# Kernel tuning notes

Measured on AMD Instinct MI355X. Metric: run time of the kernel, lower is better.

The kernel has to match this reference:

```python
import jax, jax.numpy as jnp
import numpy as np

T, D, N, K, V = 4, 1024, 256, 64, 32000
SGLD_A, SGLD_B, SGLD_C = 0.01, 1.0, 0.55
PHI_VAR, ETA_VAR = 1.0, 1.0
ZERO = 1e-6

def jax_exp(x):
    return jnp.clip(jnp.exp(jnp.clip(x, -700.0, 700.0)), ZERO)

def setup_inputs() -> dict:
    key = jax.random.key(0)
    ks = jax.random.split(key, 13)
    W = jax.random.randint(ks[0], (T, D, N), 0, V, dtype=jnp.int32)
    Z = jax.random.randint(ks[1], (T, D, N), 0, K - 1, dtype=jnp.int32)
    prop_word_idx = jax.random.randint(ks[2], (T, D, N), 0, N, dtype=jnp.int32)
    prop_topic = jax.random.randint(ks[3], (T, D, N), 0, K - 1, dtype=jnp.int32)
    u_mh = jax.random.uniform(ks[4], (T, D, N, 2), dtype=jnp.float32)
    noise_eta = jax.random.normal(ks[5], (T, D), dtype=jnp.float32)
    noise_phi = jax.random.normal(ks[6], (T,), dtype=jnp.float32)
    alpha = jax.random.normal(ks[7], (T, K), dtype=jnp.float32)
    phi = jax.random.normal(ks[8], (T, V, K), dtype=jnp.float32) * 0.1
    eta = jax.random.normal(ks[9], (T, D, K), dtype=jnp.float32) * 0.1
    CDK = jax.random.uniform(ks[10], (T, D, K), dtype=jnp.float32) * (N / K)
    CWK = jax.random.uniform(ks[11], (T, V, K), dtype=jnp.float32)
    CK = jax.random.uniform(ks[12], (T, K), dtype=jnp.float32) * (D * N / K)
    return dict(W=W, Z=Z, prop_word_idx=prop_word_idx, prop_topic=prop_topic,
                u_mh=u_mh, noise_eta=noise_eta, noise_phi=noise_phi,
                alpha=alpha, phi=phi, eta=eta, CDK=CDK, CWK=CWK, CK=CK)

def reference(W, Z, prop_word_idx, prop_topic, u_mh, noise_eta, noise_phi,
              alpha, phi, eta, CDK, CWK, CK):
    eps = SGLD_A * (SGLD_B + 0.0) ** (-SGLD_C)  # SGLD step at iteration 0

    # --- SGLD update of eta (per doc), vmapped over (T, D) via broadcasting ---
    prior_eta = (alpha[:, None, :] - eta) / ETA_VAR                 # [T,D,K]
    grad_eta = CDK - N * jax.nn.softmax(eta, axis=-1)               # [T,D,K]
    eta_new = eta + eps / 2 * (grad_eta + prior_eta) + noise_eta[..., None] * eps

    tt = jnp.arange(T)[:, None, None]   # [T,1,1]
    dd = jnp.arange(D)[None, :, None]   # [1,D,1]

    # --- MH step 1: word-proposal (acceptance via phi ratio) ---
    pre = Z                                                           # [T,D,N]
    prop1 = jnp.take_along_axis(Z, prop_word_idx, axis=2)             # [T,D,N]
    a1 = jax_exp(phi[tt, W, prop1]) / jax_exp(phi[tt, W, pre])
    k1 = jnp.where(u_mh[..., 0] < a1, prop1, pre)

    # --- MH step 2: topic-proposal (acceptance via eta ratio) ---
    a2 = jax_exp(eta_new[tt, dd, prop_topic]) / jax_exp(eta_new[tt, dd, k1])
    z_new = jnp.where(u_mh[..., 1] < a2, prop_topic, k1)              # [T,D,N]

    # --- scatter counter updates (add new assignment, remove old) ---
    CDK_new = CDK.at[tt, dd, z_new].add(1.0).at[tt, dd, Z].add(-1.0)
    CWK_new = CWK.at[tt, W, z_new].add(1.0).at[tt, W, Z].add(-1.0)
    CK_new = CK.at[tt, z_new].add(1.0).at[tt, Z].add(-1.0)

    # --- SGLD update of phi: sequential over T (reads updated phi[t-1]) ---
    rows = [phi[t] for t in range(T)]   # each [V,K]
    phi_sigma = 1.0 / (1.0 / 100.0 + 1.0 / PHI_VAR)
    for t in range(T):
        if t == 0:
            prior = (2.0 * phi[1] * (phi_sigma / PHI_VAR) - 2.0 * rows[0]) / PHI_VAR
        elif t == T - 1:
            prior = (rows[t - 1] - rows[t]) / PHI_VAR
        else:
            prior = (phi[t + 1] + rows[t - 1] - 2.0 * rows[t]) / PHI_VAR
        grad = CWK_new[t] - CK_new[t][None, :] * jax.nn.softmax(rows[t], axis=0)
        rows[t] = rows[t] + eps / 2 * (grad + prior) + noise_phi[t] * eps
    phi_new = jnp.stack(rows)

    return (eta_new, phi_new, CDK_new, CWK_new, CK_new, z_new)
```

## Files before the change

kernel.cpp:

```cpp
#include <hip/hip_runtime.h>

#define T 4
#define D 1024
#define NN 256
#define K 64
#define V 32000
#define VK (V*K)
#define TD (T*D)
#define NB 32
#define CAP 1024

__device__ __forceinline__ float jexp(float x) {
    x = fminf(fmaxf(x, -700.0f), 700.0f);
    return fmaxf(expf(x), 1e-6f);
}


__global__ void fused_kernel(const int* __restrict__ W, const int* __restrict__ Z,
                             const int* __restrict__ pwi, const int* __restrict__ ptop,
                             const float* __restrict__ u, const float* __restrict__ phi,
                             const float* __restrict__ eta,
                             const float* __restrict__ alpha,
                             const float* __restrict__ noise_eta,
                             const float* __restrict__ CDK,
                             const float* __restrict__ CK,
                             float* __restrict__ S_part,
                             float* __restrict__ CK_new,
                             float* __restrict__ eta_new,
                             float* __restrict__ CDK_new,
                             unsigned int* __restrict__ resv,
                             unsigned int* __restrict__ list,
                             float* __restrict__ z_out)
{
    int blk = blockIdx.x;
    int n = threadIdx.x;

    __shared__ float sm[256];
    __shared__ float esh[K];
    __shared__ int   hist[K];
    __shared__ int   bcnt[NB];
    __shared__ int   bbase[NB];

    if (blk < 500) {
        if (blk == 0) CK_new[n] = CK[n];
        int t = blk / 125;
        int vbase = (blk % 125) * 256;
        int k = n & 63;
        int rr = n >> 6;
        const float* base = phi + (size_t)t * VK;
        float s = 0.0f;
        #pragma unroll 4
        for (int it = 0; it < 64; ++it) {
            int v = vbase + it * 4 + rr;
            s += expf(base[v * K + k]);
        }
        sm[n] = s;
        __syncthreads();
        if (n < 64) {
            S_part[blk * 64 + n] = sm[n] + sm[n + 64] +
                                   sm[n + 128] + sm[n + 192];
        }
        return;
    }

    int b = blk - 500;
    int r = ((b & 7) << 9) | (b >> 3);
    int t = r >> 10;
    int slice = (b >> 3) & 15;

    int w     = W[r * NN + n];
    int pre   = Z[r * NN + n];
    int pw    = pwi[r * NN + n];
    int prop1 = Z[r * NN + pw];
    int pt    = ptop[r * NN + n];
    float2 uu = ((const float2*)u)[(size_t)r * NN + n];

    const float* prow = phi + ((size_t)t * V + w) * K;
    float f1 = prow[prop1];
    float f0 = prow[pre];

    float cdk = 0.0f;
    if (n < 64) {
        float x = eta[r * K + n];
        float m = x;
        #pragma unroll
        for (int off = 32; off >= 1; off >>= 1)
            m = fmaxf(m, __shfl_xor(m, off, 64));
        float e = expf(x - m);
        float s = e;
        #pragma unroll
        for (int off = 32; off >= 1; off >>= 1)
            s += __shfl_xor(s, off, 64);
        float smx = e / s;
        cdk = CDK[r * K + n];
        float grad  = cdk - (float)NN * smx;
        float prior = alpha[t * K + n] - x;
        float en = x + 0.005f * (grad + prior) + noise_eta[r] * 0.01f;
        esh[n] = en;
        eta_new[r * K + n] = en;
    } else if (n < 128) {
        hist[n - 64] = 0;
    } else if (n < 128 + NB) {
        bcnt[n - 128] = 0;
    }
    __syncthreads();

    float a1 = jexp(f1) / jexp(f0);
    int k1 = (uu.x < a1) ? prop1 : pre;

    float a2 = jexp(esh[pt]) / jexp(esh[k1]);
    int z = (uu.y < a2) ? pt : k1;

    atomicAdd(&hist[z], 1);
    atomicAdd(&hist[pre], -1);

    int keep = (z != pre);
    int bucket = w / 1000;
    int myidx = 0;
    if (keep) myidx = atomicAdd(&bcnt[bucket], 1);
    __syncthreads();

    if (n < NB) {
        bbase[n] = (int)atomicAdd(&resv[(t * NB + n) * 16 + slice],
                                  (unsigned int)bcnt[n]);
    }
    __syncthreads();

    z_out[r * NN + n] = (float)z;
    if (keep) {
        int slot = bbase[bucket] + myidx;
        if (slot < CAP) {
            unsigned int pk = (unsigned int)w | ((unsigned int)z << 15) |
                              ((unsigned int)pre << 21);
            list[(size_t)((t * NB + bucket) * 16 + slice) * CAP + slot] = pk;
        }
    }
    if (n < K) {
        CDK_new[r * K + n] = cdk + (float)hist[n];
    }
}

__global__ void cwk_kernel(const unsigned int* __restrict__ list,
                           const unsigned int* __restrict__ resv,
                           const float* __restrict__ CWK,
                           float* __restrict__ CWK_new)
{
    int b = blockIdx.x;
    int xcd    = b & 7;
    int tbh    = (b >> 3) & 15;
    int window = b >> 7;
    int tb = tbh * 8 + xcd;
    int t = tb >> 5, bucket = tb & 31;
    int vbase = bucket * 1000 + window * 125;

    __shared__ unsigned int plusH[125 * 16];
    __shared__ unsigned int minusH[125 * 16];
    for (int i = threadIdx.x; i < 2000; i += 256) { plusH[i] = 0u; minusH[i] = 0u; }
    __syncthreads();

    int wave = threadIdx.x >> 6;
    int lane = threadIdx.x & 63;
    int segbase = tb * 16;

#define DECODE(PK) {                                                        \
        int wv = (int)((PK) & 32767u);                                      \
        unsigned int vl = (unsigned int)(wv - vbase);                       \
        if (vl < 125u) {                                                    \
            int zz = (int)(((PK) >> 15) & 63u);                             \
            int pr = (int)(((PK) >> 21) & 63u);                             \
            atomicAdd(&plusH [vl * 16 + (zz >> 2)], 1u << ((zz & 3) * 8));  \
            atomicAdd(&minusH[vl * 16 + (pr >> 2)], 1u << ((pr & 3) * 8));  \
        } }

    for (int s = wave; s < 16; s += 4) {
        int len = (int)resv[segbase + s]; if (len > CAP) len = CAP;
        const unsigned int* lp = list + (size_t)(segbase + s) * CAP;
        const uint4* lp4 = (const uint4*)lp;
        int n4 = len >> 2;
        for (int i = lane; i < n4; i += 64) {
            uint4 q = lp4[i];
            DECODE(q.x); DECODE(q.y); DECODE(q.z); DECODE(q.w);
        }
        int base4 = n4 << 2;
        if (lane < (len & 3)) { unsigned int pk = lp[base4 + lane]; DECODE(pk); }
    }
#undef DECODE
    __syncthreads();

    const float4* src = (const float4*)(CWK     + ((size_t)t * V + vbase) * 64);
    float4*       dst = (float4*)      (CWK_new + ((size_t)t * V + vbase) * 64);
    for (int i4 = threadIdx.x; i4 < 2000; i4 += 256) {
        unsigned int pl = plusH[i4];
        unsigned int mi = minusH[i4];
        float4 c = src[i4];
        float4 o;
        #pragma unroll
        for (int jj = 0; jj < 4; ++jj) {
            int sh = jj * 8;
            (&o.x)[jj] = (&c.x)[jj] + (float)((pl >> sh) & 255u)
                                    - (float)((mi >> sh) & 255u);
        }
        dst[i4] = o;
    }
}

__global__ void reduce_kernel(const float* __restrict__ S_part,
                              const float* __restrict__ CDKn,
                              const float* __restrict__ CDK,
                              float* __restrict__ S,
                              float* __restrict__ CK_new)
{
    int b = blockIdx.x;
    int tid = threadIdx.x;

    if (b < 4 && tid < 64) {
        float s = 0.0f;
        #pragma unroll 5
        for (int i = 0; i < 125; ++i)
            s += S_part[(b * 125 + i) * 64 + tid];
        S[b * 64 + tid] = s;
    }

    int t  = b >> 4;
    int k  = tid & 63;
    int dl = tid >> 6;
    int dbase = (b & 15) << 6;
    float s = 0.0f;
    #pragma unroll
    for (int i = 0; i < 16; ++i) {
        int d = dbase + dl + (i << 2);
        size_t idx = ((size_t)(t << 10) + d) * 64 + k;
        s += CDKn[idx] - CDK[idx];
    }
    __shared__ float sm[256];
    sm[tid] = s;
    __syncthreads();
    if (tid < 64) {
        float tot = sm[k] + sm[k + 64] + sm[k + 128] + sm[k + 192];
        if (tot != 0.0f) atomicAdd(&CK_new[(t << 6) + k], tot);
    }
}

__global__ void phi_update_kernel(const float* __restrict__ phi,
                                  const float* __restrict__ CWKn,
                                  const float* __restrict__ CKn,
                                  const float* __restrict__ S,
                                  const float* __restrict__ noise_phi,
                                  float* __restrict__ phi_new)
{
    int i4 = blockIdx.x * 256 + threadIdx.x;
    int kg = i4 & 15;
    const float eps = 0.01f;
    const float half_eps = 0.005f;
    const float sig = 1.0f / 1.01f;

    const float4* phi4  = (const float4*)phi;
    const float4* cwk4  = (const float4*)CWKn;
    const float4* ck4   = (const float4*)CKn;
    const float4* s4    = (const float4*)S;
    float4*       out4  = (float4*)phi_new;

    float4 p0 = phi4[i4];
    float4 p1 = phi4[i4 +     512000];
    float4 p2 = phi4[i4 + 2 * 512000];
    float4 p3 = phi4[i4 + 3 * 512000];

    float4 c0 = cwk4[i4];
    float4 c1 = cwk4[i4 +     512000];
    float4 c2 = cwk4[i4 + 2 * 512000];
    float4 c3 = cwk4[i4 + 3 * 512000];

    float4 ckn0 = ck4[kg],      ckn1 = ck4[16 + kg];
    float4 ckn2 = ck4[32 + kg], ckn3 = ck4[48 + kg];
    float4 ss0 = s4[kg],        ss1 = s4[16 + kg];
    float4 ss2 = s4[32 + kg],   ss3 = s4[48 + kg];

    float np0 = noise_phi[0] * eps, np1 = noise_phi[1] * eps;
    float np2 = noise_phi[2] * eps, np3 = noise_phi[3] * eps;

    float4 o0, o1, o2, o3;
    #pragma unroll
    for (int j = 0; j < 4; ++j) {
        float q0 = (&p0.x)[j], q1 = (&p1.x)[j], q2 = (&p2.x)[j], q3 = (&p3.x)[j];
        float g0 = (&c0.x)[j] - (&ckn0.x)[j] * (expf(q0) / (&ss0.x)[j]);
        float g1 = (&c1.x)[j] - (&ckn1.x)[j] * (expf(q1) / (&ss1.x)[j]);
        float g2 = (&c2.x)[j] - (&ckn2.x)[j] * (expf(q2) / (&ss2.x)[j]);
        float g3 = (&c3.x)[j] - (&ckn3.x)[j] * (expf(q3) / (&ss3.x)[j]);

        float r0 = q0 + half_eps * (g0 + 2.0f * q1 * sig - 2.0f * q0) + np0;
        float r1 = q1 + half_eps * (g1 + q2 + r0 - 2.0f * q1)         + np1;
        float r2 = q2 + half_eps * (g2 + q3 + r1 - 2.0f * q2)         + np2;
        float r3 = q3 + half_eps * (g3 + r2 - q3)                      + np3;

        (&o0.x)[j] = r0; (&o1.x)[j] = r1; (&o2.x)[j] = r2; (&o3.x)[j] = r3;
    }

    out4[i4]              = o0;
    out4[i4 +     512000] = o1;
    out4[i4 + 2 * 512000] = o2;
    out4[i4 + 3 * 512000] = o3;
}

extern "C" void kernel_launch(void* const* d_in, const int* in_sizes, int n_in,
                              void* d_out, int out_size, void* d_ws, size_t ws_size,
                              hipStream_t stream)
{
    const int*   W         = (const int*)  d_in[0];
    const int*   Z         = (const int*)  d_in[1];
    const int*   pwi       = (const int*)  d_in[2];
    const int*   ptop      = (const int*)  d_in[3];
    const float* u_mh      = (const float*)d_in[4];
    const float* noise_eta = (const float*)d_in[5];
    const float* noise_phi = (const float*)d_in[6];
    const float* alpha     = (const float*)d_in[7];
    const float* phi       = (const float*)d_in[8];
    const float* eta       = (const float*)d_in[9];
    const float* CDK       = (const float*)d_in[10];
    const float* CWK       = (const float*)d_in[11];
    const float* CK        = (const float*)d_in[12];

    float* out     = (float*)d_out;
    float* eta_new = out;
    float* phi_new = out + 262144;
    float* CDK_new = out + 8454144;
    float* CWK_new = out + 8716288;
    float* CK_new  = out + 16908288;
    float* z_out   = out + 16908544;

    float* ws      = (float*)d_ws;
    float* S       = ws;
    float* S_part  = ws + 256;
    unsigned int* resv = (unsigned int*)(ws + 256 + 32000);
    unsigned int* list = resv + 2048;

    hipMemsetAsync(resv, 0, 2048 * sizeof(unsigned int), stream);

    fused_kernel<<<500 + TD, 256, 0, stream>>>(W, Z, pwi, ptop, u_mh, phi,
                                               eta, alpha, noise_eta, CDK, CK,
                                               S_part, CK_new,
                                               eta_new, CDK_new, resv, list, z_out);
    cwk_kernel<<<1024, 256, 0, stream>>>(list, resv, CWK, CWK_new);
    reduce_kernel<<<64, 256, 0, stream>>>(S_part, CDK_new, CDK, S, CK_new);
    phi_update_kernel<<<VK / 1024, 256, 0, stream>>>(phi, CWK_new, CK_new, S,
                                                     noise_phi, phi_new);
}
```

Before: 224.4 us.

## Fuse CWK scatter histogram with phi SGLD update into one kernel

Merges the CWK count-update kernel and the phi update kernel so each block builds histograms for all four time slices of a 125-row vocabulary window in LDS. It then applies them while computing phi, writing CWK_new without rereading it. This removes one full pass over CWK_new and a kernel launch. In exchange it uses only 256 large blocks with 64KB of LDS each, which lowers occupancy and memory-level parallelism and serializes more decode work per block.

```diff
diff --git a/kernel.cpp b/kernel.cpp
--- a/kernel.cpp
+++ b/kernel.cpp
@@ -140,70 +140,6 @@
     }
 }
 
-__global__ void cwk_kernel(const unsigned int* __restrict__ list,
-                           const unsigned int* __restrict__ resv,
-                           const float* __restrict__ CWK,
-                           float* __restrict__ CWK_new)
-{
-    int b = blockIdx.x;
-    int xcd    = b & 7;
-    int tbh    = (b >> 3) & 15;
-    int window = b >> 7;
-    int tb = tbh * 8 + xcd;
-    int t = tb >> 5, bucket = tb & 31;
-    int vbase = bucket * 1000 + window * 125;
-
-    __shared__ unsigned int plusH[125 * 16];
-    __shared__ unsigned int minusH[125 * 16];
-    for (int i = threadIdx.x; i < 2000; i += 256) { plusH[i] = 0u; minusH[i] = 0u; }
-    __syncthreads();
-
-    int wave = threadIdx.x >> 6;
-    int lane = threadIdx.x & 63;
-    int segbase = tb * 16;
-
-#define DECODE(PK) {                                                        \
-        int wv = (int)((PK) & 32767u);                                      \
-        unsigned int vl = (unsigned int)(wv - vbase);                       \
-        if (vl < 125u) {                                                    \
-            int zz = (int)(((PK) >> 15) & 63u);                             \
-            int pr = (int)(((PK) >> 21) & 63u);                             \
-            atomicAdd(&plusH [vl * 16 + (zz >> 2)], 1u << ((zz & 3) * 8));  \
-            atomicAdd(&minusH[vl * 16 + (pr >> 2)], 1u << ((pr & 3) * 8));  \
-        } }
-
-    for (int s = wave; s < 16; s += 4) {
-        int len = (int)resv[segbase + s]; if (len > CAP) len = CAP;
-        const unsigned int* lp = list + (size_t)(segbase + s) * CAP;
-        const uint4* lp4 = (const uint4*)lp;
-        int n4 = len >> 2;
-        for (int i = lane; i < n4; i += 64) {
-            uint4 q = lp4[i];
-            DECODE(q.x); DECODE(q.y); DECODE(q.z); DECODE(q.w);
-        }
-        int base4 = n4 << 2;
-        if (lane < (len & 3)) { unsigned int pk = lp[base4 + lane]; DECODE(pk); }
-    }
-#undef DECODE
-    __syncthreads();
-
-    const float4* src = (const float4*)(CWK     + ((size_t)t * V + vbase) * 64);
-    float4*       dst = (float4*)      (CWK_new + ((size_t)t * V + vbase) * 64);
-    for (int i4 = threadIdx.x; i4 < 2000; i4 += 256) {
-        unsigned int pl = plusH[i4];
-        unsigned int mi = minusH[i4];
-        float4 c = src[i4];
-        float4 o;
-        #pragma unroll
-        for (int jj = 0; jj < 4; ++jj) {
-            int sh = jj * 8;
-            (&o.x)[jj] = (&c.x)[jj] + (float)((pl >> sh) & 255u)
-                                    - (float)((mi >> sh) & 255u);
-        }
-        dst[i4] = o;
-    }
-}
-
 __global__ void reduce_kernel(const float* __restrict__ S_part,
                               const float* __restrict__ CDKn,
                               const float* __restrict__ CDK,
@@ -241,64 +177,134 @@
     }
 }
 
-__global__ void phi_update_kernel(const float* __restrict__ phi,
-                                  const float* __restrict__ CWKn,
-                                  const float* __restrict__ CKn,
-                                  const float* __restrict__ S,
-                                  const float* __restrict__ noise_phi,
-                                  float* __restrict__ phi_new)
+__global__ void cwkphi_kernel(const unsigned int* __restrict__ list,
+                              const unsigned int* __restrict__ resv,
+                              const float* __restrict__ CWK,
+                              const float* __restrict__ phi,
+                              const float* __restrict__ CKn,
+                              const float* __restrict__ S,
+                              const float* __restrict__ noise_phi,
+                              float* __restrict__ CWK_new,
+                              float* __restrict__ phi_new)
 {
-    int i4 = blockIdx.x * 256 + threadIdx.x;
-    int kg = i4 & 15;
+    int b = blockIdx.x;
+    int bucket = b & 31;
+    int window = b >> 5;
+    int vbase = bucket * 1000 + window * 125;
+
+    __shared__ unsigned int plusH[4][2000];
+    __shared__ unsigned int minusH[4][2000];
+    for (int i = threadIdx.x; i < 2000; i += 256) {
+        plusH[0][i] = 0u; plusH[1][i] = 0u; plusH[2][i] = 0u; plusH[3][i] = 0u;
+        minusH[0][i] = 0u; minusH[1][i] = 0u; minusH[2][i] = 0u; minusH[3][i] = 0u;
+    }
+    __syncthreads();
+
+    int wave = threadIdx.x >> 6;
+    int lane = threadIdx.x & 63;
+
+#define DECODE(PK, TT) {                                                          \
+        int wv = (int)((PK) & 32767u);                                            \
+        unsigned int vl = (unsigned int)(wv - vbase);                             \
+        if (vl < 125u) {                                                          \
+            int zz = (int)(((PK) >> 15) & 63u);                                   \
+            int pr = (int)(((PK) >> 21) & 63u);                                   \
+            atomicAdd(&plusH [TT][vl * 16 + (zz >> 2)], 1u << ((zz & 3) * 8));    \
+            atomicAdd(&minusH[TT][vl * 16 + (pr >> 2)], 1u << ((pr & 3) * 8));    \
+        } }
+
+    for (int ss = wave; ss < 64; ss += 4) {
+        int t = ss >> 4;
+        int s = ss & 15;
+        int seg = (t * NB + bucket) * 16 + s;
+        int len = (int)resv[seg]; if (len > CAP) len = CAP;
+        const unsigned int* lp = list + (size_t)seg * CAP;
+        const uint4* lp4 = (const uint4*)lp;
+        int n4 = len >> 2;
+        for (int i = lane; i < n4; i += 64) {
+            uint4 q = lp4[i];
+            DECODE(q.x, t); DECODE(q.y, t); DECODE(q.z, t); DECODE(q.w, t);
+        }
+        int base4 = n4 << 2;
+        if (lane < (len & 3)) { unsigned int pk = lp[base4 + lane]; DECODE(pk, t); }
+    }
+#undef DECODE
+    __syncthreads();
+
     const float eps = 0.01f;
     const float half_eps = 0.005f;
     const float sig = 1.0f / 1.01f;
 
     const float4* phi4  = (const float4*)phi;
-    const float4* cwk4  = (const float4*)CWKn;
+    const float4* cwk4  = (const float4*)CWK;
     const float4* ck4   = (const float4*)CKn;
     const float4* s4    = (const float4*)S;
-    float4*       out4  = (float4*)phi_new;
-
-    float4 p0 = phi4[i4];
-    float4 p1 = phi4[i4 +     512000];
-    float4 p2 = phi4[i4 + 2 * 512000];
-    float4 p3 = phi4[i4 + 3 * 512000];
-
-    float4 c0 = cwk4[i4];
-    float4 c1 = cwk4[i4 +     512000];
-    float4 c2 = cwk4[i4 + 2 * 512000];
-    float4 c3 = cwk4[i4 + 3 * 512000];
-
-    float4 ckn0 = ck4[kg],      ckn1 = ck4[16 + kg];
-    float4 ckn2 = ck4[32 + kg], ckn3 = ck4[48 + kg];
-    float4 ss0 = s4[kg],        ss1 = s4[16 + kg];
-    float4 ss2 = s4[32 + kg],   ss3 = s4[48 + kg];
+    float4*       pout4 = (float4*)phi_new;
+    float4*       cout4 = (float4*)CWK_new;
 
     float np0 = noise_phi[0] * eps, np1 = noise_phi[1] * eps;
     float np2 = noise_phi[2] * eps, np3 = noise_phi[3] * eps;
 
-    float4 o0, o1, o2, o3;
-    #pragma unroll
-    for (int j = 0; j < 4; ++j) {
-        float q0 = (&p0.x)[j], q1 = (&p1.x)[j], q2 = (&p2.x)[j], q3 = (&p3.x)[j];
-        float g0 = (&c0.x)[j] - (&ckn0.x)[j] * (expf(q0) / (&ss0.x)[j]);
-        float g1 = (&c1.x)[j] - (&ckn1.x)[j] * (expf(q1) / (&ss1.x)[j]);
-        float g2 = (&c2.x)[j] - (&ckn2.x)[j] * (expf(q2) / (&ss2.x)[j]);
-        float g3 = (&c3.x)[j] - (&ckn3.x)[j] * (expf(q3) / (&ss3.x)[j]);
-
-        float r0 = q0 + half_eps * (g0 + 2.0f * q1 * sig - 2.0f * q0) + np0;
-        float r1 = q1 + half_eps * (g1 + q2 + r0 - 2.0f * q1)         + np1;
-        float r2 = q2 + half_eps * (g2 + q3 + r1 - 2.0f * q2)         + np2;
-        float r3 = q3 + half_eps * (g3 + r2 - q3)                      + np3;
-
-        (&o0.x)[j] = r0; (&o1.x)[j] = r1; (&o2.x)[j] = r2; (&o3.x)[j] = r3;
-    }
-
-    out4[i4]              = o0;
-    out4[i4 +     512000] = o1;
-    out4[i4 + 2 * 512000] = o2;
-    out4[i4 + 3 * 512000] = o3;
+    size_t base4 = (size_t)vbase * 16;
+
+    for (int i4 = threadIdx.x; i4 < 2000; i4 += 256) {
+        int kg = i4 & 15;
+        size_t g = base4 + i4;
+
+        float4 p0 = phi4[g];
+        float4 p1 = phi4[g +     512000];
+        float4 p2 = phi4[g + 2 * 512000];
+        float4 p3 = phi4[g + 3 * 512000];
+
+        float4 c0 = cwk4[g];
+        float4 c1 = cwk4[g +     512000];
+        float4 c2 = cwk4[g + 2 * 512000];
+        float4 c3 = cwk4[g + 3 * 512000];
+
+        unsigned int pl0 = plusH[0][i4], mi0 = minusH[0][i4];
+        unsigned int pl1 = plusH[1][i4], mi1 = minusH[1][i4];
+        unsigned int pl2 = plusH[2][i4], mi2 = minusH[2][i4];
+        unsigned int pl3 = plusH[3][i4], mi3 = minusH[3][i4];
+
+        float4 ckn0 = ck4[kg],      ckn1 = ck4[16 + kg];
+        float4 ckn2 = ck4[32 + kg], ckn3 = ck4[48 + kg];
+        float4 ss0 = s4[kg],        ss1 = s4[16 + kg];
+        float4 ss2 = s4[32 + kg],   ss3 = s4[48 + kg];
+
+        float4 o0, o1, o2, o3, w0, w1, w2, w3;
+        #pragma unroll
+        for (int j = 0; j < 4; ++j) {
+            int sh = j * 8;
+            float q0 = (&p0.x)[j], q1 = (&p1.x)[j], q2 = (&p2.x)[j], q3 = (&p3.x)[j];
+            float cw0 = (&c0.x)[j] + (float)((pl0 >> sh) & 255u) - (float)((mi0 >> sh) & 255u);
+            float cw1 = (&c1.x)[j] + (float)((pl1 >> sh) & 255u) - (float)((mi1 >> sh) & 255u);
+            float cw2 = (&c2.x)[j] + (float)((pl2 >> sh) & 255u) - (float)((mi2 >> sh) & 255u);
+            float cw3 = (&c3.x)[j] + (float)((pl3 >> sh) & 255u) - (float)((mi3 >> sh) & 255u);
+            (&w0.x)[j] = cw0; (&w1.x)[j] = cw1; (&w2.x)[j] = cw2; (&w3.x)[j] = cw3;
+
+            float g0 = cw0 - (&ckn0.x)[j] * (expf(q0) / (&ss0.x)[j]);
+            float g1 = cw1 - (&ckn1.x)[j] * (expf(q1) / (&ss1.x)[j]);
+            float g2 = cw2 - (&ckn2.x)[j] * (expf(q2) / (&ss2.x)[j]);
+            float g3 = cw3 - (&ckn3.x)[j] * (expf(q3) / (&ss3.x)[j]);
+
+            float r0 = q0 + half_eps * (g0 + 2.0f * q1 * sig - 2.0f * q0) + np0;
+            float r1 = q1 + half_eps * (g1 + q2 + r0 - 2.0f * q1)         + np1;
+            float r2 = q2 + half_eps * (g2 + q3 + r1 - 2.0f * q2)         + np2;
+            float r3 = q3 + half_eps * (g3 + r2 - q3)                      + np3;
+
+            (&o0.x)[j] = r0; (&o1.x)[j] = r1; (&o2.x)[j] = r2; (&o3.x)[j] = r3;
+        }
+
+        pout4[g]              = o0;
+        pout4[g +     512000] = o1;
+        pout4[g + 2 * 512000] = o2;
+        pout4[g + 3 * 512000] = o3;
+
+        cout4[g]              = w0;
+        cout4[g +     512000] = w1;
+        cout4[g + 2 * 512000] = w2;
+        cout4[g + 3 * 512000] = w3;
+    }
 }
 
 extern "C" void kernel_launch(void* const* d_in, const int* in_sizes, int n_in,
@@ -339,8 +345,7 @@
                                                eta, alpha, noise_eta, CDK, CK,
                                                S_part, CK_new,
                                                eta_new, CDK_new, resv, list, z_out);
-    cwk_kernel<<<1024, 256, 0, stream>>>(list, resv, CWK, CWK_new);
     reduce_kernel<<<64, 256, 0, stream>>>(S_part, CDK_new, CDK, S, CK_new);
-    phi_update_kernel<<<VK / 1024, 256, 0, stream>>>(phi, CWK_new, CK_new, S,
-                                                     noise_phi, phi_new);
-}
+    cwkphi_kernel<<<256, 256, 0, stream>>>(list, resv, CWK, phi, CK_new, S,
+                                           noise_phi, CWK_new, phi_new);
+}
```

Result: slower. 245.0 us (+9.2%).
